# Kernel tuning notes

Hardware: AMD Instinct MI355X
Metric: run time of the kernel (lower is better)

The kernel has to match this reference:

```python
import jax, jax.numpy as jnp
from jax import lax
import numpy as np

B = 32        # graphs per batch
NN = 513      # nodes per graph (odd M so Y/Z head lengths match)
IN = 128      # input_dim
OUT = 256     # output_dim
T = 4         # edge_types
STEPS = 4     # ggnn propagation steps
DEG = 16
N = B * NN
E = N * DEG
CAT = IN + OUT


def setup_inputs() -> dict:
    key = jax.random.key(0)
    ks = jax.random.split(key, 16)
    f32 = jnp.float32
    feature = jax.random.normal(ks[0], (N, IN), f32)
    offs = (jnp.arange(B) * NN)[:, None]
    edge_src = (jax.random.randint(ks[1], (B, NN * DEG), 0, NN) + offs).reshape(-1)
    edge_dst = (jax.random.randint(ks[2], (B, NN * DEG), 0, NN) + offs).reshape(-1)
    edge_type = jax.random.randint(ks[3], (E,), 0, T)
    s = 1.0 / np.sqrt(OUT)
    W_msg = jax.random.normal(ks[4], (T, OUT, OUT), f32) * s      # [T, out, in] (torch Linear layout)
    b_msg = jnp.zeros((T, OUT), f32)
    gru_w_ih = jax.random.normal(ks[5], (3 * OUT, OUT), f32) * s
    gru_w_hh = jax.random.normal(ks[6], (3 * OUT, OUT), f32) * s
    gru_b_ih = jnp.zeros((3 * OUT,), f32)
    gru_b_hh = jnp.zeros((3 * OUT,), f32)
    conv1_w = jax.random.normal(ks[7], (OUT, OUT, 3), f32) * (1.0 / np.sqrt(OUT * 3))
    conv1_b = jnp.zeros((OUT,), f32)
    conv2_w = jax.random.normal(ks[8], (OUT, OUT, 1), f32) * s
    conv2_b = jnp.zeros((OUT,), f32)
    convc1_w = jax.random.normal(ks[9], (CAT, CAT, 3), f32) * (1.0 / np.sqrt(CAT * 3))
    convc1_b = jnp.zeros((CAT,), f32)
    convc2_w = jax.random.normal(ks[10], (CAT, CAT, 2), f32) * (1.0 / np.sqrt(CAT * 2))
    convc2_b = jnp.zeros((CAT,), f32)
    mlpy_w = jax.random.normal(ks[11], (1, OUT), f32) * s
    mlpy_b = jnp.zeros((1,), f32)
    mlpz_w = jax.random.normal(ks[12], (1, CAT), f32) * (1.0 / np.sqrt(CAT))
    mlpz_b = jnp.zeros((1,), f32)
    return dict(feature=feature, W_msg=W_msg, b_msg=b_msg,
                gru_w_ih=gru_w_ih, gru_w_hh=gru_w_hh, gru_b_ih=gru_b_ih, gru_b_hh=gru_b_hh,
                conv1_w=conv1_w, conv1_b=conv1_b, conv2_w=conv2_w, conv2_b=conv2_b,
                convc1_w=convc1_w, convc1_b=convc1_b, convc2_w=convc2_w, convc2_b=convc2_b,
                mlpy_w=mlpy_w, mlpy_b=mlpy_b, mlpz_w=mlpz_w, mlpz_b=mlpz_b,
                edge_src=edge_src, edge_dst=edge_dst, edge_type=edge_type)


def _conv1d(x, w, b):
    # x: [B, C_in, L], w: [C_out, C_in, K]
    y = lax.conv_general_dilated(x, w, (1,), 'VALID', dimension_numbers=('NCH', 'OIH', 'NCH'))
    return y + b[None, :, None]


def _maxpool1d(x, k, s):
    init = jnp.array(-jnp.inf, dtype=x.dtype)
    return lax.reduce_window(x, init, lax.max, (1, 1, k), (1, 1, s), 'VALID')


def _forward(feature, W_msg, b_msg, gru_w_ih, gru_w_hh, gru_b_ih, gru_b_hh,
             conv1_w, conv1_b, conv2_w, conv2_b, convc1_w, convc1_b, convc2_w, convc2_b,
             mlpy_w, mlpy_b, mlpz_w, mlpz_b, edge_src, edge_dst, edge_type):
    # --- GatedGraphConv (DGL semantics): zero-pad features to out_feats ---
    h = jnp.pad(feature, ((0, 0), (0, OUT - IN)))  # [N, OUT]
    for _ in range(STEPS):
        # per-etype linear on all nodes: hw[t] = h @ W_msg[t].T + b_msg[t]
        hw = jnp.einsum('nd,tod->tno', h, W_msg) + b_msg[:, None, :]   # [T, N, OUT]
        msg = hw[edge_type, edge_src]                                   # [E, OUT] gather
        a = jax.ops.segment_sum(msg, edge_dst, num_segments=N)          # [N, OUT] scatter-add
        # GRUCell(a, h) in torch gate order (r, z, n)
        gi = a @ gru_w_ih.T + gru_b_ih
        gh = h @ gru_w_hh.T + gru_b_hh
        ir, iz, inn = jnp.split(gi, 3, axis=-1)
        hr, hz, hn = jnp.split(gh, 3, axis=-1)
        r = jax.nn.sigmoid(ir + hr)
        z = jax.nn.sigmoid(iz + hz)
        n = jnp.tanh(inn + r * hn)
        h = (1.0 - z) * n + z * h
    outputs = h                                             # [N, OUT]
    ci = jnp.concatenate([outputs, feature], axis=-1)       # [N, OUT+IN]
    # batchify to [B, C, L]
    hi = outputs.reshape(B, NN, OUT).transpose(0, 2, 1)
    cb = ci.reshape(B, NN, CAT).transpose(0, 2, 1)
    Y1 = _maxpool1d(jax.nn.relu(_conv1d(hi, conv1_w, conv1_b)), 3, 2)
    Y2 = _maxpool1d(jax.nn.relu(_conv1d(Y1, conv2_w, conv2_b)), 2, 2).transpose(0, 2, 1)   # [B, 127, OUT]
    Z1 = _maxpool1d(jax.nn.relu(_conv1d(cb, convc1_w, convc1_b)), 3, 2)
    Z2 = _maxpool1d(jax.nn.relu(_conv1d(Z1, convc2_w, convc2_b)), 2, 2).transpose(0, 2, 1)  # [B, 127, CAT]
    before_avg = (Y2 @ mlpy_w.T + mlpy_b) * (Z2 @ mlpz_w.T + mlpz_b)   # [B, 127, 1]
    avg = before_avg.mean(axis=1)                                       # [B, 1]
    return jax.nn.sigmoid(avg).squeeze(-1)                              # [B]


def reference(feature, W_msg, b_msg, gru_w_ih, gru_w_hh, gru_b_ih, gru_b_hh,
              conv1_w, conv1_b, conv2_w, conv2_b, convc1_w, convc1_b, convc2_w, convc2_b,
              mlpy_w, mlpy_b, mlpz_w, mlpz_b, edge_src, edge_dst, edge_type):
    return _forward(feature, W_msg, b_msg, gru_w_ih, gru_w_hh, gru_b_ih, gru_b_hh,
                    conv1_w, conv1_b, conv2_w, conv2_b, convc1_w, convc1_b, convc2_w, convc2_b,
                    mlpy_w, mlpy_b, mlpz_w, mlpz_b, edge_src, edge_dst, edge_type)
```

## Files before the change

kernel.cpp:

```cpp
#include <hip/hip_runtime.h>

#define Bg    32
#define NNg   513
#define INF   128
#define OUTF  256
#define TT    4
#define NSTEP 4
#define DEGg  16
#define Ntot  (Bg*NNg)
#define Etot  (Ntot*DEGg)
#define CATF  (OUTF+INF)
#define SK    1056

typedef _Float16 h8_t __attribute__((ext_vector_type(8)));
typedef float    f4_t __attribute__((ext_vector_type(4)));

__global__ void pad_h_k(const float* __restrict__ feat, float* __restrict__ h,
                        _Float16* __restrict__ h16) {
  int idx = blockIdx.x*256 + threadIdx.x;
  if (idx >= Ntot*OUTF) return;
  int n = idx >> 8, c = idx & 255;
  float v = (c < INF) ? feat[n*INF + c] : 0.f;
  h[idx] = v;
  h16[idx] = (_Float16)v;
}

__global__ void cvt_k(const float* __restrict__ s, _Float16* __restrict__ d, int n) {
  int i = (blockIdx.x*256 + threadIdx.x) * 4;
  if (i >= n) return;
  float4 v = *reinterpret_cast<const float4*>(s + i);
  _Float16 o[4] = {(_Float16)v.x, (_Float16)v.y, (_Float16)v.z, (_Float16)v.w};
  *reinterpret_cast<ushort4*>(d + i) = *reinterpret_cast<ushort4*>(o);
}

__global__ void build_cb16_k(const _Float16* __restrict__ h16,
                             const float* __restrict__ feat,
                             _Float16* __restrict__ cb) {
  int idx = blockIdx.x*256 + threadIdx.x;
  if (idx >= Ntot*CATF) return;
  int n = idx / CATF, c = idx % CATF;
  cb[idx] = (c < OUTF) ? h16[n*OUTF + c] : (_Float16)feat[n*INF + (c - OUTF)];
}

__global__ void zero_int_k(int* __restrict__ p, int n) {
  int i = blockIdx.x*256 + threadIdx.x;
  if (i < n) p[i] = 0;
}

__global__ void hist_k(const int* __restrict__ dst, int* __restrict__ cnt) {
  int e = blockIdx.x*256 + threadIdx.x;
  if (e < Etot) atomicAdd(&cnt[dst[e]], 1);
}

__global__ void scan_k(const int* __restrict__ cnt, int* __restrict__ rowptr) {
  __shared__ int buf[256];
  __shared__ int carry_s;
  if (threadIdx.x == 0) carry_s = 0;
  __syncthreads();
  for (int base = 0; base < Ntot; base += 256) {
    int i = base + threadIdx.x;
    int v = (i < Ntot) ? cnt[i] : 0;
    buf[threadIdx.x] = v;
    __syncthreads();
    #pragma unroll
    for (int off = 1; off < 256; off <<= 1) {
      int t = (threadIdx.x >= off) ? buf[threadIdx.x - off] : 0;
      __syncthreads();
      buf[threadIdx.x] += t;
      __syncthreads();
    }
    if (i < Ntot) rowptr[i] = carry_s + buf[threadIdx.x] - v;
    __syncthreads();
    if (threadIdx.x == 255) carry_s += buf[255];
    __syncthreads();
  }
  if (threadIdx.x == 0) rowptr[Ntot] = carry_s;
}

__global__ void fill_k(const int* __restrict__ dst, const int* __restrict__ rowptr,
                       int* __restrict__ cursor, int* __restrict__ eidx) {
  int e = blockIdx.x*256 + threadIdx.x;
  if (e < Etot) {
    int d = dst[e];
    int pos = atomicAdd(&cursor[d], 1);
    eidx[rowptr[d] + pos] = e;
  }
}

__global__ void gather_k(const _Float16* __restrict__ h16, const int* __restrict__ rowptr,
                         const int* __restrict__ eidx, const int* __restrict__ esrc,
                         const int* __restrict__ etyp, _Float16* __restrict__ s16) {
  __shared__ int src_s[128];
  __shared__ int typ_s[128];
  int n = blockIdx.x;
  int c = threadIdx.x;
  int s0 = rowptr[n], e0 = rowptr[n+1];
  float a0 = 0.f, a1 = 0.f, a2 = 0.f, a3 = 0.f;
  int c0 = 0, c1 = 0, c2 = 0, c3 = 0;
  for (int base = s0; base < e0; base += 128) {
    int m = e0 - base; if (m > 128) m = 128;
    if (c < m) {
      int ee = eidx[base + c];
      src_s[c] = esrc[ee];
      typ_s[c] = etyp[ee];
    }
    __syncthreads();
    for (int i = 0; i < m; ++i) {
      int t = typ_s[i];
      float v = (float)h16[(size_t)src_s[i]*256 + c];
      a0 += (t == 0) ? v : 0.f;
      a1 += (t == 1) ? v : 0.f;
      a2 += (t == 2) ? v : 0.f;
      a3 += (t == 3) ? v : 0.f;
      c0 += (t == 0); c1 += (t == 1); c2 += (t == 2); c3 += (t == 3);
    }
    __syncthreads();
  }
  size_t b = (size_t)n * SK;
  s16[b + 0*256 + c] = (_Float16)a0;
  s16[b + 1*256 + c] = (_Float16)a1;
  s16[b + 2*256 + c] = (_Float16)a2;
  s16[b + 3*256 + c] = (_Float16)a3;
  if (c < 32) {
    float cv = (c == 0) ? (float)c0 : (c == 1) ? (float)c1 :
               (c == 2) ? (float)c2 : (c == 3) ? (float)c3 : 0.f;
    s16[b + 1024 + c] = (_Float16)cv;
  }
}

__global__ void repack_wext_k(const float* __restrict__ Wmsg, const float* __restrict__ bmsg,
                              _Float16* __restrict__ wext) {
  int idx = blockIdx.x*256 + threadIdx.x;
  if (idx >= 256*SK) return;
  int co = idx / SK, k = idx % SK;
  float v;
  if (k < 1024)      { int t = k >> 8, ci = k & 255; v = Wmsg[((size_t)t*256 + co)*256 + ci]; }
  else if (k < 1028) { v = bmsg[(k - 1024)*256 + co]; }
  else               { v = 0.f; }
  wext[idx] = (_Float16)v;
}

__global__ void gru_gate_k(const float* __restrict__ gi, const float* __restrict__ gh,
                           float* __restrict__ h, _Float16* __restrict__ h16) {
  int idx = blockIdx.x*256 + threadIdx.x;
  if (idx >= Ntot*OUTF) return;
  int n = idx >> 8, g = idx & 255;
  const float* gin = gi + (size_t)n*768;
  const float* ghn = gh + (size_t)n*768;
  float r  = 1.f / (1.f + expf(-(gin[g]       + ghn[g])));
  float z  = 1.f / (1.f + expf(-(gin[256 + g] + ghn[256 + g])));
  float nn = tanhf(gin[512 + g] + r * ghn[512 + g]);
  float hv = h[idx];
  float o = (1.f - z) * nn + z * hv;
  h[idx] = o;
  h16[idx] = (_Float16)o;
}

template<typename OT>
__global__ void maxpool_k(const float* __restrict__ in, OT* __restrict__ out,
                          int Lin, int Lp, int C, int kwin) {
  int idx = blockIdx.x*256 + threadIdx.x;
  int total = Bg*Lp*C;
  if (idx >= total) return;
  int c = idx % C; int r = idx / C; int p = r % Lp; int b = r / Lp;
  const float* base = in + ((size_t)(b*Lin + 2*p))*C + c;
  float v = base[0];
  for (int w = 1; w < kwin; ++w) v = fmaxf(v, base[(size_t)w*C]);
  out[idx] = (OT)v;
}

__global__ void repack16_k(const float* __restrict__ w, _Float16* __restrict__ wk,
                           int Cout, int Cin, int K) {
  int idx = blockIdx.x*256 + threadIdx.x;
  int total = Cout*Cin*K;
  if (idx >= total) return;
  int ci = idx % Cin; int r = idx / Cin; int k = r % K; int co = r / K;
  wk[idx] = (_Float16)w[(co*Cin + ci)*K + k];
}

__global__ void head_k(const float* __restrict__ Y2, const float* __restrict__ Z2,
                       const float* __restrict__ wy, const float* __restrict__ by,
                       const float* __restrict__ wz, const float* __restrict__ bz,
                       float* __restrict__ out) {
  int b = blockIdx.x;
  int tid = threadIdx.x;
  __shared__ float red[128];
  float sum = 0.f;
  for (int p = tid; p < 127; p += 128) {
    const float* yr = Y2 + ((size_t)(b*127 + p))*OUTF;
    const float* zr = Z2 + ((size_t)(b*127 + p))*CATF;
    float yv = by[0], zv = bz[0];
    for (int c = 0; c < OUTF; ++c) yv = fmaf(yr[c], wy[c], yv);
    for (int c = 0; c < CATF; ++c) zv = fmaf(zr[c], wz[c], zv);
    sum += yv * zv;
  }
  red[tid] = sum;
  __syncthreads();
  for (int off = 64; off > 0; off >>= 1) {
    if (tid < off) red[tid] += red[tid + off];
    __syncthreads();
  }
  if (tid == 0) out[b] = 1.f / (1.f + expf(-red[0] / 127.f));
}

template<typename CT, bool RELU, bool MAPPED>
__global__ __launch_bounds__(256, 2) void hgemm(
    const _Float16* __restrict__ A, const _Float16* __restrict__ W,
    const float* __restrict__ bias, CT* __restrict__ C,
    int M, int Nout, int K, int arstride, int Lout, int NNodes) {
  __shared__ _Float16 As[128][40];
  __shared__ _Float16 Ws[64][40];
  int tid = threadIdx.x;
  int lane = tid & 63, wid = tid >> 6;
  int wm = wid >> 1, wn = wid & 1;
  int l15 = lane & 15, l4 = lane >> 4;
  int m0 = blockIdx.x * 128, n0 = blockIdx.y * 64;

  int sa_row = tid >> 1;
  int sa_col = (tid & 1) * 16;
  int m_s = m0 + sa_row;
  bool a_ok = (m_s < M);
  int mc = a_ok ? m_s : (M - 1);
  int node = MAPPED ? (mc / Lout) * NNodes + (mc % Lout) : mc;
  const _Float16* a_src = A + (size_t)node * arstride + sa_col;
  int sw_row = tid >> 2;
  int sw_col = (tid & 3) * 8;
  const _Float16* w_src = W + (size_t)(n0 + sw_row) * K + sw_col;

  f4_t acc[4][2] = {};

  for (int k0 = 0; k0 < K; k0 += 32) {
    if (k0) __syncthreads();
    int4 v0 = {0,0,0,0}, v1 = {0,0,0,0};
    if (a_ok) {
      const int4* g = reinterpret_cast<const int4*>(a_src + k0);
      v0 = g[0]; v1 = g[1];
    }
    *reinterpret_cast<int4*>(&As[sa_row][sa_col])     = v0;
    *reinterpret_cast<int4*>(&As[sa_row][sa_col + 8]) = v1;
    *reinterpret_cast<int4*>(&Ws[sw_row][sw_col]) =
        *reinterpret_cast<const int4*>(w_src + k0);
    __syncthreads();

    h8_t af[4], bf[2];
    #pragma unroll
    for (int fm = 0; fm < 4; ++fm)
      af[fm] = *reinterpret_cast<const h8_t*>(&As[wm*64 + fm*16 + l15][l4*8]);
    #pragma unroll
    for (int fn = 0; fn < 2; ++fn)
      bf[fn] = *reinterpret_cast<const h8_t*>(&Ws[wn*32 + fn*16 + l15][l4*8]);
    #pragma unroll
    for (int fm = 0; fm < 4; ++fm)
      #pragma unroll
      for (int fn = 0; fn < 2; ++fn)
        acc[fm][fn] = __builtin_amdgcn_mfma_f32_16x16x32_f16(af[fm], bf[fn], acc[fm][fn], 0, 0, 0);
  }

  #pragma unroll
  for (int fn = 0; fn < 2; ++fn) {
    int col = n0 + wn*32 + fn*16 + l15;
    float bv = bias[col];
    #pragma unroll
    for (int fm = 0; fm < 4; ++fm) {
      #pragma unroll
      for (int i = 0; i < 4; ++i) {
        int m = m0 + wm*64 + fm*16 + l4*4 + i;
        if (m >= M) continue;
        float v = acc[fm][fn][i] + bv;
        if (RELU) v = fmaxf(v, 0.f);
        C[(size_t)m * Nout + col] = (CT)v;
      }
    }
  }
}

static inline int cdiv(int x, int y) { return (x + y - 1) / y; }

extern "C" void kernel_launch(void* const* d_in, const int* in_sizes, int n_in,
                              void* d_out, int out_size, void* d_ws, size_t ws_size,
                              hipStream_t stream) {
  const float* feature  = (const float*)d_in[0];
  const float* W_msg    = (const float*)d_in[1];
  const float* b_msg    = (const float*)d_in[2];
  const float* w_ih     = (const float*)d_in[3];
  const float* w_hh     = (const float*)d_in[4];
  const float* b_ih     = (const float*)d_in[5];
  const float* b_hh     = (const float*)d_in[6];
  const float* conv1_w  = (const float*)d_in[7];
  const float* conv1_b  = (const float*)d_in[8];
  const float* conv2_w  = (const float*)d_in[9];
  const float* conv2_b  = (const float*)d_in[10];
  const float* convc1_w = (const float*)d_in[11];
  const float* convc1_b = (const float*)d_in[12];
  const float* convc2_w = (const float*)d_in[13];
  const float* convc2_b = (const float*)d_in[14];
  const float* mlpy_w   = (const float*)d_in[15];
  const float* mlpy_b   = (const float*)d_in[16];
  const float* mlpz_w   = (const float*)d_in[17];
  const float* mlpz_b   = (const float*)d_in[18];
  const int*   esrc     = (const int*)d_in[19];
  const int*   edst     = (const int*)d_in[20];
  const int*   etyp     = (const int*)d_in[21];
  float* out = (float*)d_out;

  char* base = (char*)d_ws;
  size_t off = 0;
  auto alloc = [&](size_t bytes) { void* p = base + off; off = (off + bytes + 255) & ~(size_t)255; return p; };
  float*    h      = (float*)   alloc((size_t)Ntot*OUTF*4);
  _Float16* h16    = (_Float16*)alloc((size_t)Ntot*OUTF*2);
  _Float16* Wext16 = (_Float16*)alloc((size_t)256*SK*2);
  _Float16* wih16  = (_Float16*)alloc((size_t)768*256*2);
  _Float16* whh16  = (_Float16*)alloc((size_t)768*256*2);
  float*    bias0  = (float*)   alloc(256*4);
  int* rowptr = (int*)alloc((Ntot+1)*4);
  int* cnt    = (int*)alloc(Ntot*4);
  int* eidx   = (int*)alloc((size_t)Etot*4);
  char* big   = (char*)alloc((size_t)Ntot*1536*4);
  float*    gi  = (float*)big;
  float*    gh  = gi + (size_t)Ntot*768;
  _Float16* s16 = (_Float16*)(big + (size_t)Ntot*768*4);
  _Float16* a16 = s16 + (size_t)Ntot*SK;
  float*    Y2   = (float*)big;
  float*    Z2   = Y2 + (size_t)Bg*127*OUTF;
  float*    y1   = Z2 + (size_t)Bg*127*CATF;
  float*    y2   = y1 + (size_t)Bg*511*OUTF;
  _Float16* p1   = (_Float16*)(y2 + (size_t)Bg*255*OUTF);
  _Float16* cb16 = p1 + (size_t)Bg*255*OUTF;
  float*    z1   = (float*)(cb16 + (size_t)Ntot*CATF);
  float*    z2   = z1 + (size_t)Bg*511*CATF;
  _Float16* pz1  = (_Float16*)(z2 + (size_t)Bg*254*CATF);
  _Float16* wk1  = pz1 + (size_t)Bg*255*CATF;
  _Float16* wkc1 = wk1 + (size_t)256*768;
  _Float16* wkc2 = wkc1 + (size_t)384*1152;
  _Float16* c2w16= wkc2 + (size_t)384*768;

  dim3 blk(256);

  pad_h_k<<<cdiv(Ntot*OUTF,256), blk, 0, stream>>>(feature, h, h16);
  repack_wext_k<<<cdiv(256*SK,256), blk, 0, stream>>>(W_msg, b_msg, Wext16);
  cvt_k<<<cdiv(768*256/4,256), blk, 0, stream>>>(w_ih, wih16, 768*256);
  cvt_k<<<cdiv(768*256/4,256), blk, 0, stream>>>(w_hh, whh16, 768*256);
  hipMemsetAsync(bias0, 0, 256*4, stream);

  zero_int_k<<<cdiv(Ntot,256), blk, 0, stream>>>(cnt, Ntot);
  hist_k<<<cdiv(Etot,256), blk, 0, stream>>>(edst, cnt);
  scan_k<<<1, blk, 0, stream>>>(cnt, rowptr);
  zero_int_k<<<cdiv(Ntot,256), blk, 0, stream>>>(cnt, Ntot);
  fill_k<<<cdiv(Etot,256), blk, 0, stream>>>(edst, rowptr, cnt, eidx);

  for (int s = 0; s < NSTEP; ++s) {
    gather_k<<<Ntot, blk, 0, stream>>>(h16, rowptr, eidx, esrc, etyp, s16);
    hgemm<_Float16,false,false><<<dim3(cdiv(Ntot,128), 4), blk, 0, stream>>>(
        s16, Wext16, bias0, a16, Ntot, 256, SK, SK, 0, 0);
    hgemm<float,false,false><<<dim3(cdiv(Ntot,128), 12), blk, 0, stream>>>(
        a16, wih16, b_ih, gi, Ntot, 768, 256, 256, 0, 0);
    hgemm<float,false,false><<<dim3(cdiv(Ntot,128), 12), blk, 0, stream>>>(
        h16, whh16, b_hh, gh, Ntot, 768, 256, 256, 0, 0);
    gru_gate_k<<<cdiv(Ntot*OUTF,256), blk, 0, stream>>>(gi, gh, h, h16);
  }

  repack16_k<<<cdiv(256*256*3,256), blk, 0, stream>>>(conv1_w,  wk1,  256, 256, 3);
  repack16_k<<<cdiv(384*384*3,256), blk, 0, stream>>>(convc1_w, wkc1, 384, 384, 3);
  repack16_k<<<cdiv(384*384*2,256), blk, 0, stream>>>(convc2_w, wkc2, 384, 384, 2);
  cvt_k<<<cdiv(256*256/4,256), blk, 0, stream>>>(conv2_w, c2w16, 256*256);

  hgemm<float,true,true><<<dim3(cdiv(Bg*511,128), 4), blk, 0, stream>>>(
      h16, wk1, conv1_b, y1, Bg*511, 256, 768, 256, 511, NNg);
  maxpool_k<_Float16><<<cdiv(Bg*255*256,256), blk, 0, stream>>>(y1, p1, 511, 255, 256, 3);
  hgemm<float,true,false><<<dim3(cdiv(Bg*255,128), 4), blk, 0, stream>>>(
      p1, c2w16, conv2_b, y2, Bg*255, 256, 256, 256, 0, 0);
  maxpool_k<float><<<cdiv(Bg*127*256,256), blk, 0, stream>>>(y2, Y2, 255, 127, 256, 2);

  build_cb16_k<<<cdiv(Ntot*CATF,256), blk, 0, stream>>>(h16, feature, cb16);
  hgemm<float,true,true><<<dim3(cdiv(Bg*511,128), 6), blk, 0, stream>>>(
      cb16, wkc1, convc1_b, z1, Bg*511, 384, 1152, 384, 511, NNg);
  maxpool_k<_Float16><<<cdiv(Bg*255*384,256), blk, 0, stream>>>(z1, pz1, 511, 255, 384, 3);
  hgemm<float,true,true><<<dim3(cdiv(Bg*254,128), 6), blk, 0, stream>>>(
      pz1, wkc2, convc2_b, z2, Bg*254, 384, 768, 384, 254, 255);
  maxpool_k<float><<<cdiv(Bg*127*384,256), blk, 0, stream>>>(z2, Z2, 254, 127, 384, 2);

  head_k<<<Bg, 128, 0, stream>>>(Y2, Z2, mlpy_w, mlpy_b, mlpz_w, mlpz_b, out);
}
```

Before: 972.6 us.

## Widen GEMM N-tile to 128 and parallelize CSR prefix scan

The hgemm tile grows from 128x64 to 128x128, so each wave computes a 64x64 sub-tile with 16 MFMA accumulators. This halves the grid in the N dimension and raises arithmetic intensity per LDS load of the A tile. The single-block serial prefix scan is replaced by a three-kernel block scan: per-block scan, scan of block sums, then add-back. The trade-off is more accumulator registers, which may hurt occupancy under launch_bounds(256,2), and fewer blocks for the smaller conv GEMMs.

```diff
diff --git a/kernel.cpp b/kernel.cpp
--- a/kernel.cpp
+++ b/kernel.cpp
@@ -11,6 +11,7 @@
 #define Etot  (Ntot*DEGg)
 #define CATF  (OUTF+INF)
 #define SK    1056
+#define NSB   65
 
 typedef _Float16 h8_t __attribute__((ext_vector_type(8)));
 typedef float    f4_t __attribute__((ext_vector_type(4)));
@@ -52,29 +53,45 @@
   if (e < Etot) atomicAdd(&cnt[dst[e]], 1);
 }
 
-__global__ void scan_k(const int* __restrict__ cnt, int* __restrict__ rowptr) {
+__global__ void scan1_k(const int* __restrict__ cnt, int* __restrict__ rowptr,
+                        int* __restrict__ bsum) {
   __shared__ int buf[256];
-  __shared__ int carry_s;
-  if (threadIdx.x == 0) carry_s = 0;
+  int t = threadIdx.x;
+  int i = blockIdx.x*256 + t;
+  int v = (i < Ntot) ? cnt[i] : 0;
+  buf[t] = v;
   __syncthreads();
-  for (int base = 0; base < Ntot; base += 256) {
-    int i = base + threadIdx.x;
-    int v = (i < Ntot) ? cnt[i] : 0;
-    buf[threadIdx.x] = v;
-    __syncthreads();
-    #pragma unroll
-    for (int off = 1; off < 256; off <<= 1) {
-      int t = (threadIdx.x >= off) ? buf[threadIdx.x - off] : 0;
-      __syncthreads();
-      buf[threadIdx.x] += t;
-      __syncthreads();
-    }
-    if (i < Ntot) rowptr[i] = carry_s + buf[threadIdx.x] - v;
-    __syncthreads();
-    if (threadIdx.x == 255) carry_s += buf[255];
-    __syncthreads();
-  }
-  if (threadIdx.x == 0) rowptr[Ntot] = carry_s;
+  #pragma unroll
+  for (int off = 1; off < 256; off <<= 1) {
+    int x = (t >= off) ? buf[t - off] : 0;
+    __syncthreads();
+    buf[t] += x;
+    __syncthreads();
+  }
+  if (i < Ntot) rowptr[i] = buf[t] - v;
+  if (t == 255) bsum[blockIdx.x] = buf[255];
+}
+
+__global__ void scan2_k(int* __restrict__ bsum) {
+  __shared__ int buf[256];
+  int t = threadIdx.x;
+  int v = (t < NSB) ? bsum[t] : 0;
+  buf[t] = v;
+  __syncthreads();
+  #pragma unroll
+  for (int off = 1; off < 256; off <<= 1) {
+    int x = (t >= off) ? buf[t - off] : 0;
+    __syncthreads();
+    buf[t] += x;
+    __syncthreads();
+  }
+  if (t < NSB) bsum[t] = buf[t] - v;
+}
+
+__global__ void scan3_k(int* __restrict__ rowptr, const int* __restrict__ bsum) {
+  int i = blockIdx.x*256 + threadIdx.x;
+  if (i < Ntot) rowptr[i] += bsum[blockIdx.x];
+  if (i == 0) rowptr[Ntot] = Etot;
 }
 
 __global__ void fill_k(const int* __restrict__ dst, const int* __restrict__ rowptr,
@@ -209,56 +226,56 @@
     const float* __restrict__ bias, CT* __restrict__ C,
     int M, int Nout, int K, int arstride, int Lout, int NNodes) {
   __shared__ _Float16 As[128][40];
-  __shared__ _Float16 Ws[64][40];
+  __shared__ _Float16 Ws[128][40];
   int tid = threadIdx.x;
   int lane = tid & 63, wid = tid >> 6;
   int wm = wid >> 1, wn = wid & 1;
   int l15 = lane & 15, l4 = lane >> 4;
-  int m0 = blockIdx.x * 128, n0 = blockIdx.y * 64;
-
-  int sa_row = tid >> 1;
-  int sa_col = (tid & 1) * 16;
-  int m_s = m0 + sa_row;
+  int m0 = blockIdx.x * 128, n0 = blockIdx.y * 128;
+
+  int s_row = tid >> 1;
+  int s_col = (tid & 1) * 16;
+  int m_s = m0 + s_row;
   bool a_ok = (m_s < M);
   int mc = a_ok ? m_s : (M - 1);
   int node = MAPPED ? (mc / Lout) * NNodes + (mc % Lout) : mc;
-  const _Float16* a_src = A + (size_t)node * arstride + sa_col;
-  int sw_row = tid >> 2;
-  int sw_col = (tid & 3) * 8;
-  const _Float16* w_src = W + (size_t)(n0 + sw_row) * K + sw_col;
-
-  f4_t acc[4][2] = {};
+  const _Float16* a_src = A + (size_t)node * arstride + s_col;
+  const _Float16* w_src = W + (size_t)(n0 + s_row) * K + s_col;
+
+  f4_t acc[4][4] = {};
 
   for (int k0 = 0; k0 < K; k0 += 32) {
     if (k0) __syncthreads();
-    int4 v0 = {0,0,0,0}, v1 = {0,0,0,0};
+    int4 va0 = {0,0,0,0}, va1 = {0,0,0,0};
     if (a_ok) {
-      const int4* g = reinterpret_cast<const int4*>(a_src + k0);
-      v0 = g[0]; v1 = g[1];
+      const int4* ga = reinterpret_cast<const int4*>(a_src + k0);
+      va0 = ga[0]; va1 = ga[1];
     }
-    *reinterpret_cast<int4*>(&As[sa_row][sa_col])     = v0;
-    *reinterpret_cast<int4*>(&As[sa_row][sa_col + 8]) = v1;
-    *reinterpret_cast<int4*>(&Ws[sw_row][sw_col]) =
-        *reinterpret_cast<const int4*>(w_src + k0);
-    __syncthreads();
-
-    h8_t af[4], bf[2];
+    const int4* gw = reinterpret_cast<const int4*>(w_src + k0);
+    int4 vw0 = gw[0], vw1 = gw[1];
+    *reinterpret_cast<int4*>(&As[s_row][s_col])     = va0;
+    *reinterpret_cast<int4*>(&As[s_row][s_col + 8]) = va1;
+    *reinterpret_cast<int4*>(&Ws[s_row][s_col])     = vw0;
+    *reinterpret_cast<int4*>(&Ws[s_row][s_col + 8]) = vw1;
+    __syncthreads();
+
+    h8_t af[4], bf[4];
     #pragma unroll
     for (int fm = 0; fm < 4; ++fm)
       af[fm] = *reinterpret_cast<const h8_t*>(&As[wm*64 + fm*16 + l15][l4*8]);
     #pragma unroll
-    for (int fn = 0; fn < 2; ++fn)
-      bf[fn] = *reinterpret_cast<const h8_t*>(&Ws[wn*32 + fn*16 + l15][l4*8]);
+    for (int fn = 0; fn < 4; ++fn)
+      bf[fn] = *reinterpret_cast<const h8_t*>(&Ws[wn*64 + fn*16 + l15][l4*8]);
     #pragma unroll
     for (int fm = 0; fm < 4; ++fm)
       #pragma unroll
-      for (int fn = 0; fn < 2; ++fn)
+      for (int fn = 0; fn < 4; ++fn)
         acc[fm][fn] = __builtin_amdgcn_mfma_f32_16x16x32_f16(af[fm], bf[fn], acc[fm][fn], 0, 0, 0);
   }
 
   #pragma unroll
-  for (int fn = 0; fn < 2; ++fn) {
-    int col = n0 + wn*32 + fn*16 + l15;
+  for (int fn = 0; fn < 4; ++fn) {
+    int col = n0 + wn*64 + fn*16 + l15;
     float bv = bias[col];
     #pragma unroll
     for (int fm = 0; fm < 4; ++fm) {
@@ -314,6 +331,7 @@
   float*    bias0  = (float*)   alloc(256*4);
   int* rowptr = (int*)alloc((Ntot+1)*4);
   int* cnt    = (int*)alloc(Ntot*4);
+  int* bsum   = (int*)alloc(NSB*4);
   int* eidx   = (int*)alloc((size_t)Etot*4);
   char* big   = (char*)alloc((size_t)Ntot*1536*4);
   float*    gi  = (float*)big;
@@ -344,17 +362,19 @@
 
   zero_int_k<<<cdiv(Ntot,256), blk, 0, stream>>>(cnt, Ntot);
   hist_k<<<cdiv(Etot,256), blk, 0, stream>>>(edst, cnt);
-  scan_k<<<1, blk, 0, stream>>>(cnt, rowptr);
+  scan1_k<<<NSB, blk, 0, stream>>>(cnt, rowptr, bsum);
+  scan2_k<<<1, blk, 0, stream>>>(bsum);
+  scan3_k<<<NSB, blk, 0, stream>>>(rowptr, bsum);
   zero_int_k<<<cdiv(Ntot,256), blk, 0, stream>>>(cnt, Ntot);
   fill_k<<<cdiv(Etot,256), blk, 0, stream>>>(edst, rowptr, cnt, eidx);
 
   for (int s = 0; s < NSTEP; ++s) {
     gather_k<<<Ntot, blk, 0, stream>>>(h16, rowptr, eidx, esrc, etyp, s16);
-    hgemm<_Float16,false,false><<<dim3(cdiv(Ntot,128), 4), blk, 0, stream>>>(
+    hgemm<_Float16,false,false><<<dim3(cdiv(Ntot,128), 2), blk, 0, stream>>>(
         s16, Wext16, bias0, a16, Ntot, 256, SK, SK, 0, 0);
-    hgemm<float,false,false><<<dim3(cdiv(Ntot,128), 12), blk, 0, stream>>>(
+    hgemm<float,false,false><<<dim3(cdiv(Ntot,128), 6), blk, 0, stream>>>(
         a16, wih16, b_ih, gi, Ntot, 768, 256, 256, 0, 0);
-    hgemm<float,false,false><<<dim3(cdiv(Ntot,128), 12), blk, 0, stream>>>(
+    hgemm<float,false,false><<<dim3(cdiv(Ntot,128), 6), blk, 0, stream>>>(
         h16, whh16, b_hh, gh, Ntot, 768, 256, 256, 0, 0);
     gru_gate_k<<<cdiv(Ntot*OUTF,256), blk, 0, stream>>>(gi, gh, h, h16);
   }
@@ -364,18 +384,18 @@
   repack16_k<<<cdiv(384*384*2,256), blk, 0, stream>>>(convc2_w, wkc2, 384, 384, 2);
   cvt_k<<<cdiv(256*256/4,256), blk, 0, stream>>>(conv2_w, c2w16, 256*256);
 
-  hgemm<float,true,true><<<dim3(cdiv(Bg*511,128), 4), blk, 0, stream>>>(
+  hgemm<float,true,true><<<dim3(cdiv(Bg*511,128), 2), blk, 0, stream>>>(
       h16, wk1, conv1_b, y1, Bg*511, 256, 768, 256, 511, NNg);
   maxpool_k<_Float16><<<cdiv(Bg*255*256,256), blk, 0, stream>>>(y1, p1, 511, 255, 256, 3);
-  hgemm<float,true,false><<<dim3(cdiv(Bg*255,128), 4), blk, 0, stream>>>(
+  hgemm<float,true,false><<<dim3(cdiv(Bg*255,128), 2), blk, 0, stream>>>(
       p1, c2w16, conv2_b, y2, Bg*255, 256, 256, 256, 0, 0);
   maxpool_k<float><<<cdiv(Bg*127*256,256), blk, 0, stream>>>(y2, Y2, 255, 127, 256, 2);
 
   build_cb16_k<<<cdiv(Ntot*CATF,256), blk, 0, stream>>>(h16, feature, cb16);
-  hgemm<float,true,true><<<dim3(cdiv(Bg*511,128), 6), blk, 0, stream>>>(
+  hgemm<float,true,true><<<dim3(cdiv(Bg*511,128), 3), blk, 0, stream>>>(
       cb16, wkc1, convc1_b, z1, Bg*511, 384, 1152, 384, 511, NNg);
   maxpool_k<_Float16><<<cdiv(Bg*255*384,256), blk, 0, stream>>>(z1, pz1, 511, 255, 384, 3);
-  hgemm<float,true,true><<<dim3(cdiv(Bg*254,128), 6), blk, 0, stream>>>(
+  hgemm<float,true,true><<<dim3(cdiv(Bg*254,128), 3), blk, 0, stream>>>(
       pz1, wkc2, convc2_b, z2, Bg*254, 384, 768, 384, 254, 255);
   maxpool_k<float><<<cdiv(Bg*127*384,256), blk, 0, stream>>>(z2, Z2, 254, 127, 384, 2);
 
```

After: 896.8 us. -7.8%, faster.
